# Kernel optimization log

Hardware: AMD Instinct MI355X
Metric: run time of the kernel (lower is better)

Reference implementation:

```python
import jax, jax.numpy as jnp
import numpy as np

N, E, R, D = 50000, 100000, 64, 50


def setup_inputs() -> dict:
    key = jax.random.key(0)
    k0, k1, k2, k3, k4 = jax.random.split(key, 5)
    h = jax.random.normal(k0, (N, D), dtype=jnp.float32)
    # xavier_uniform with gain=sqrt(2) (relu): bound = gain*sqrt(6/(fan_in+fan_out))
    bound = np.sqrt(2.0) * np.sqrt(6.0 / (D + D))
    weight = jax.random.uniform(k1, (R, D, D), dtype=jnp.float32, minval=-bound, maxval=bound)
    bias = jnp.ones((D,), dtype=jnp.float32)
    src_idx = jax.random.randint(k2, (E,), 0, N)
    dst_idx = jax.random.randint(k3, (E,), 0, N)
    rel_type = jax.random.randint(k4, (E,), 0, R)
    return {"h": h, "weight": weight, "bias": bias,
            "src_idx": src_idx, "dst_idx": dst_idx, "rel_type": rel_type}


def reference(h, weight, bias, src_idx, dst_idx, rel_type):
    # message_func: per-edge relation weight gather + bmm with source features
    # h[src_idx]: [E, D], weight[rel_type]: [E, D, D] -> msg: [E, D]
    msg = jnp.einsum('ed,edk->ek', h[src_idx], weight[rel_type])
    # sum-reduce messages onto destination nodes (DGL fn.sum semantics)
    agg = jax.ops.segment_sum(msg, dst_idx, num_segments=N)
    # apply_func: bias add + ReLU on node features
    return jax.nn.relu(agg + bias)
```

## Files before the change

kernel.cpp:

```cpp
#include <hip/hip_runtime.h>

#define NN 50000
#define DD 50
#define RR 64
#define BINS 2048
#define CAP 128
#define CAPN 24

#define BINCUR_OFF 0
#define DCUR_OFF   2048
#define PERM_OFF   52048
#define SD_OFF     1252048
#define META_INTS  1776336
#define WB_BYTE    ((size_t)META_INTS * 4)
#define MSG_BYTE   (WB_BYTE + (size_t)RR * 64 * 64 * 2)
#define WS_NEED    (MSG_BYTE + (size_t)BINS * CAP * 64 * 2)

typedef __attribute__((ext_vector_type(8))) short bf16x8;
typedef __attribute__((ext_vector_type(4))) float f32x4;

__device__ __forceinline__ unsigned short f2b(float f) {
    unsigned u = __float_as_uint(f);
    u = (u + 0x7fffu + ((u >> 16) & 1u)) >> 16;
    return (unsigned short)u;
}

__global__ __launch_bounds__(256) void k_zero(int* __restrict__ meta) {
    int i = blockIdx.x * 256 + threadIdx.x;
    if (i < BINS) meta[i] = 0;
}

__device__ __forceinline__ void load_a(const float* __restrict__ hrow, int ch,
                                       bf16x8& a0, bf16x8& a1) {
    const float2* hp0 = (const float2*)(hrow + ch * 8);
    float2 q0 = hp0[0], q1 = hp0[1], q2 = hp0[2], q3 = hp0[3];
    int kb = 32 + ch * 8;
    const float2 z2 = make_float2(0.f, 0.f);
    float2 q4 = (kb + 1 < DD) ? *(const float2*)(hrow + kb)     : z2;
    float2 q5 = (kb + 3 < DD) ? *(const float2*)(hrow + kb + 2) : z2;
    float2 q6 = (kb + 5 < DD) ? *(const float2*)(hrow + kb + 4) : z2;
    float2 q7 = (kb + 7 < DD) ? *(const float2*)(hrow + kb + 6) : z2;
    a0[0] = f2b(q0.x); a0[1] = f2b(q0.y); a0[2] = f2b(q1.x); a0[3] = f2b(q1.y);
    a0[4] = f2b(q2.x); a0[5] = f2b(q2.y); a0[6] = f2b(q3.x); a0[7] = f2b(q3.y);
    a1[0] = f2b(q4.x); a1[1] = f2b(q4.y); a1[2] = f2b(q5.x); a1[3] = f2b(q5.y);
    a1[4] = f2b(q6.x); a1[5] = f2b(q6.y); a1[6] = f2b(q7.x); a1[7] = f2b(q7.y);
}

__global__ __launch_bounds__(256) void k_prep(int* __restrict__ meta,
        unsigned short* __restrict__ wb, const float* __restrict__ w,
        const int* __restrict__ src, const int* __restrict__ dst,
        const int* __restrict__ rel, int E) {
    int tid = blockIdx.x * 256 + threadIdx.x;
    int nth = gridDim.x * 256;
    for (int j = tid; j < NN; j += nth) meta[DCUR_OFF + j] = 0;
    for (int j = tid; j < RR * 64 * 64; j += nth) {
        int r = j >> 12, d = (j >> 6) & 63, n = j & 63;
        float v = (n < DD && d < DD) ? w[r * (DD * DD) + d * DD + n] : 0.f;
        wb[(r << 12) + (n << 6) + d] = f2b(v);
    }
    for (int e = tid; e < E; e += nth) {
        int sb = (rel[e] << 5) | (e & 31);
        int p = atomicAdd(&meta[BINCUR_OFF + sb], 1);
        if (p < CAP)
            ((int2*)(meta + SD_OFF))[sb * CAP + p] = make_int2(src[e], dst[e]);
    }
}

__global__ __launch_bounds__(256) void k_edge(const float* __restrict__ h,
        const unsigned short* __restrict__ wb, int* __restrict__ meta,
        unsigned short* __restrict__ msg) {
    int lane = threadIdx.x & 63;
    int wv = (blockIdx.x << 2) + (threadIdx.x >> 6);
    int b = wv >> 2, qt = wv & 3;
    int r = b >> 5;
    int ch = lane >> 4, col0 = lane & 15;
    int slotbase = (b << 7) + (qt << 5);

    const unsigned short* wr = wb + ((size_t)r << 12) + (col0 << 6) + (ch << 3);
    bf16x8 bb0[4], bb1[4];
    #pragma unroll
    for (int t = 0; t < 4; ++t) {
        bb0[t] = *(const bf16x8*)(wr + t * 1024);
        bb1[t] = *(const bf16x8*)(wr + t * 1024 + 32);
    }

    int cnt = __builtin_amdgcn_readfirstlane(meta[BINCUR_OFF + b]);
    int2 sd = ((const int2*)(meta + SD_OFF))[slotbase + lane];
    if (cnt > CAP) cnt = CAP;
    int avail = cnt - (qt << 5);
    if (avail <= 0) return;
    if (avail > 32) avail = 32;

    int svx = (lane < avail) ? sd.x : 0;
    int sv0 = __shfl(svx, col0);
    int sv1 = __shfl(svx, 16 + col0);
    bf16x8 a00, a01, a10, a11;
    load_a(h + (size_t)sv0 * DD, ch, a00, a01);
    load_a(h + (size_t)sv1 * DD, ch, a10, a11);

    if (lane < avail) {
        int pos = atomicAdd(&meta[DCUR_OFF + sd.y], 1);
        if (pos < CAPN)
            meta[PERM_OFF + sd.y * CAPN + pos] = slotbase + lane;
    }

    {
        f32x4 c[4];
        #pragma unroll
        for (int t = 0; t < 4; ++t) {
            c[t] = (f32x4){0.f, 0.f, 0.f, 0.f};
            c[t] = __builtin_amdgcn_mfma_f32_16x16x32_bf16(a00, bb0[t], c[t], 0, 0, 0);
            c[t] = __builtin_amdgcn_mfma_f32_16x16x32_bf16(a01, bb1[t], c[t], 0, 0, 0);
        }
        unsigned short* mb = msg + (size_t)(slotbase + (ch << 2)) * 64;
        #pragma unroll
        for (int q = 0; q < 4; ++q)
            #pragma unroll
            for (int t = 0; t < 4; ++t)
                mb[q * 64 + t * 16 + col0] = f2b(c[t][q]);
    }
    if (avail > 16) {
        f32x4 c[4];
        #pragma unroll
        for (int t = 0; t < 4; ++t) {
            c[t] = (f32x4){0.f, 0.f, 0.f, 0.f};
            c[t] = __builtin_amdgcn_mfma_f32_16x16x32_bf16(a10, bb0[t], c[t], 0, 0, 0);
            c[t] = __builtin_amdgcn_mfma_f32_16x16x32_bf16(a11, bb1[t], c[t], 0, 0, 0);
        }
        unsigned short* mb = msg + (size_t)(slotbase + 16 + (ch << 2)) * 64;
        #pragma unroll
        for (int q = 0; q < 4; ++q)
            #pragma unroll
            for (int t = 0; t < 4; ++t)
                mb[q * 64 + t * 16 + col0] = f2b(c[t][q]);
    }
}

__global__ __launch_bounds__(256) void k_agg(const unsigned short* __restrict__ msg,
        const int* __restrict__ meta, const float* __restrict__ bias,
        float* __restrict__ out) {
    int lane = threadIdx.x & 63;
    int n0 = ((blockIdx.x << 2) + (threadIdx.x >> 6)) << 1;
    if (n0 >= NN) return;
    float bl = (lane < DD) ? bias[lane] : 0.f;
    #pragma unroll
    for (int ni = 0; ni < 2; ++ni) {
        int n = n0 + ni;
        if (n >= NN) break;
        int cnt = __builtin_amdgcn_readfirstlane(meta[DCUR_OFF + n]);
        if (cnt > CAPN) cnt = CAPN;
        float v = 0.f;
        const int4* pp = (const int4*)(meta + PERM_OFF + n * CAPN);
        int4 P0 = pp[0], P1 = pp[1];
        int pj[8] = {P0.x, P0.y, P0.z, P0.w, P1.x, P1.y, P1.z, P1.w};
        #pragma unroll
        for (int j = 0; j < 8; ++j) {
            if (j < cnt) {
                unsigned short u = msg[(size_t)pj[j] * 64 + lane];
                v += __uint_as_float((unsigned)u << 16);
            }
        }
        #pragma unroll 1
        for (int j = 8; j < cnt; ++j) {
            int p = meta[PERM_OFF + n * CAPN + j];
            unsigned short u = msg[(size_t)p * 64 + lane];
            v += __uint_as_float((unsigned)u << 16);
        }
        if (lane < DD) {
            float o = v + bl;
            out[(size_t)n * DD + lane] = o > 0.f ? o : 0.f;
        }
    }
}

__global__ void fb_edge_kernel(const float* __restrict__ h, const float* __restrict__ weight,
                               const int* __restrict__ src_idx, const int* __restrict__ dst_idx,
                               const int* __restrict__ rel_type, float* __restrict__ acc, int E) {
    int wave = (int)((blockIdx.x * blockDim.x + threadIdx.x) >> 6);
    int lane = threadIdx.x & 63;
    if (wave >= E) return;
    int s = src_idx[wave], r = rel_type[wave], dn = dst_idx[wave];
    const float* hs = h + (size_t)s * DD;
    const float* W  = weight + (size_t)r * DD * DD;
    if (lane < DD) {
        float m = 0.f;
        for (int d = 0; d < DD; ++d) m = fmaf(hs[d], W[d * DD + lane], m);
        atomicAdd(&acc[(size_t)dn * DD + lane], m);
    }
}
__global__ void fb_zero_kernel(float* __restrict__ out, int total) {
    int i = blockIdx.x * blockDim.x + threadIdx.x;
    if (i < total) out[i] = 0.f;
}
__global__ void fb_finalize_kernel(float* __restrict__ out, const float* __restrict__ bias, int total) {
    int i = blockIdx.x * blockDim.x + threadIdx.x;
    if (i < total) {
        float v = out[i] + bias[i % DD];
        out[i] = v > 0.f ? v : 0.f;
    }
}

extern "C" void kernel_launch(void* const* d_in, const int* in_sizes, int n_in,
                              void* d_out, int out_size, void* d_ws, size_t ws_size,
                              hipStream_t stream) {
    const float* h      = (const float*)d_in[0];
    const float* weight = (const float*)d_in[1];
    const float* bias   = (const float*)d_in[2];
    const int*   src    = (const int*)d_in[3];
    const int*   dst    = (const int*)d_in[4];
    const int*   rel    = (const int*)d_in[5];
    float* out = (float*)d_out;
    int E = in_sizes[3];

    if (ws_size >= WS_NEED) {
        int* meta = (int*)d_ws;
        unsigned short* wb  = (unsigned short*)((char*)d_ws + WB_BYTE);
        unsigned short* msg = (unsigned short*)((char*)d_ws + MSG_BYTE);

        k_zero<<<(BINS + 255) / 256, 256, 0, stream>>>(meta);
        k_prep<<<1024, 256, 0, stream>>>(meta, wb, weight, src, dst, rel, E);
        k_edge<<<2048, 256, 0, stream>>>(h, wb, meta, msg);
        k_agg<<<(NN + 7) / 8, 256, 0, stream>>>(msg, meta, bias, out);
    } else {
        fb_zero_kernel<<<(out_size + 255) / 256, 256, 0, stream>>>(out, out_size);
        fb_edge_kernel<<<(E + 3) / 4, 256, 0, stream>>>(h, weight, src, dst, rel, out, E);
        fb_finalize_kernel<<<(out_size + 255) / 256, 256, 0, stream>>>(out, bias, out_size);
    }
}
```

Before: 58.89 us.

## Scatter edge messages directly into per-destination slots, removing permutation indirection

The edge kernel now writes each message row straight into a destination-major buffer (dst*CAPN+pos) instead of writing to a bin-slot buffer and recording a permutation. The aggregation kernel then reads contiguous per-node message rows with no index lookup. The wave-to-bin mapping is also changed so that consecutive waves cover different bins, and the source-row gathers are issued before the count check to hide their latency. The cost is scattered 128-byte stores in the edge kernel and a much larger message buffer (NN*CAPN rows), which raises the workspace requirement.

```diff
diff --git a/kernel.cpp b/kernel.cpp
--- a/kernel.cpp
+++ b/kernel.cpp
@@ -9,12 +9,11 @@
 
 #define BINCUR_OFF 0
 #define DCUR_OFF   2048
-#define PERM_OFF   52048
-#define SD_OFF     1252048
-#define META_INTS  1776336
+#define SD_OFF     52048
+#define META_INTS  576336
 #define WB_BYTE    ((size_t)META_INTS * 4)
 #define MSG_BYTE   (WB_BYTE + (size_t)RR * 64 * 64 * 2)
-#define WS_NEED    (MSG_BYTE + (size_t)BINS * CAP * 64 * 2)
+#define WS_NEED    (MSG_BYTE + (size_t)NN * CAPN * 64 * 2)
 
 typedef __attribute__((ext_vector_type(8))) short bf16x8;
 typedef __attribute__((ext_vector_type(4))) float f32x4;
@@ -68,10 +67,10 @@
 
 __global__ __launch_bounds__(256) void k_edge(const float* __restrict__ h,
         const unsigned short* __restrict__ wb, int* __restrict__ meta,
-        unsigned short* __restrict__ msg) {
+        unsigned short* __restrict__ msgD) {
     int lane = threadIdx.x & 63;
     int wv = (blockIdx.x << 2) + (threadIdx.x >> 6);
-    int b = wv >> 2, qt = wv & 3;
+    int b = wv & (BINS - 1), qt = wv >> 11;
     int r = b >> 5;
     int ch = lane >> 4, col0 = lane & 15;
     int slotbase = (b << 7) + (qt << 5);
@@ -84,24 +83,23 @@
         bb1[t] = *(const bf16x8*)(wr + t * 1024 + 32);
     }
 
+    int2 sd = ((const int2*)(meta + SD_OFF))[slotbase + lane];
+    int svc = sd.x; svc = (svc < 0 || svc >= NN) ? 0 : svc;
+    int sv0 = __shfl(svc, col0);
+    int sv1 = __shfl(svc, 16 + col0);
+    bf16x8 a00, a01, a10, a11;
+    load_a(h + (size_t)sv0 * DD, ch, a00, a01);
+    load_a(h + (size_t)sv1 * DD, ch, a10, a11);
+
     int cnt = __builtin_amdgcn_readfirstlane(meta[BINCUR_OFF + b]);
-    int2 sd = ((const int2*)(meta + SD_OFF))[slotbase + lane];
     if (cnt > CAP) cnt = CAP;
     int avail = cnt - (qt << 5);
     if (avail <= 0) return;
     if (avail > 32) avail = 32;
 
-    int svx = (lane < avail) ? sd.x : 0;
-    int sv0 = __shfl(svx, col0);
-    int sv1 = __shfl(svx, 16 + col0);
-    bf16x8 a00, a01, a10, a11;
-    load_a(h + (size_t)sv0 * DD, ch, a00, a01);
-    load_a(h + (size_t)sv1 * DD, ch, a10, a11);
-
+    int pos = -1;
     if (lane < avail) {
-        int pos = atomicAdd(&meta[DCUR_OFF + sd.y], 1);
-        if (pos < CAPN)
-            meta[PERM_OFF + sd.y * CAPN + pos] = slotbase + lane;
+        pos = atomicAdd(&meta[DCUR_OFF + sd.y], 1);
     }
 
     {
@@ -112,12 +110,18 @@
             c[t] = __builtin_amdgcn_mfma_f32_16x16x32_bf16(a00, bb0[t], c[t], 0, 0, 0);
             c[t] = __builtin_amdgcn_mfma_f32_16x16x32_bf16(a01, bb1[t], c[t], 0, 0, 0);
         }
-        unsigned short* mb = msg + (size_t)(slotbase + (ch << 2)) * 64;
-        #pragma unroll
-        for (int q = 0; q < 4; ++q)
-            #pragma unroll
-            for (int t = 0; t < 4; ++t)
-                mb[q * 64 + t * 16 + col0] = f2b(c[t][q]);
+        #pragma unroll
+        for (int q = 0; q < 4; ++q) {
+            int rw = (ch << 2) + q;
+            int dvq  = __shfl(sd.y, rw);
+            int posq = __shfl(pos, rw);
+            if (rw < avail && posq >= 0 && posq < CAPN) {
+                unsigned short* mb = msgD + (size_t)(dvq * CAPN + posq) * 64;
+                #pragma unroll
+                for (int t = 0; t < 4; ++t)
+                    mb[t * 16 + col0] = f2b(c[t][q]);
+            }
+        }
     }
     if (avail > 16) {
         f32x4 c[4];
@@ -127,16 +131,22 @@
             c[t] = __builtin_amdgcn_mfma_f32_16x16x32_bf16(a10, bb0[t], c[t], 0, 0, 0);
             c[t] = __builtin_amdgcn_mfma_f32_16x16x32_bf16(a11, bb1[t], c[t], 0, 0, 0);
         }
-        unsigned short* mb = msg + (size_t)(slotbase + 16 + (ch << 2)) * 64;
-        #pragma unroll
-        for (int q = 0; q < 4; ++q)
-            #pragma unroll
-            for (int t = 0; t < 4; ++t)
-                mb[q * 64 + t * 16 + col0] = f2b(c[t][q]);
-    }
-}
-
-__global__ __launch_bounds__(256) void k_agg(const unsigned short* __restrict__ msg,
+        #pragma unroll
+        for (int q = 0; q < 4; ++q) {
+            int rw = 16 + (ch << 2) + q;
+            int dvq  = __shfl(sd.y, rw);
+            int posq = __shfl(pos, rw);
+            if (rw < avail && posq >= 0 && posq < CAPN) {
+                unsigned short* mb = msgD + (size_t)(dvq * CAPN + posq) * 64;
+                #pragma unroll
+                for (int t = 0; t < 4; ++t)
+                    mb[t * 16 + col0] = f2b(c[t][q]);
+            }
+        }
+    }
+}
+
+__global__ __launch_bounds__(256) void k_agg(const unsigned short* __restrict__ msgD,
         const int* __restrict__ meta, const float* __restrict__ bias,
         float* __restrict__ out) {
     int lane = threadIdx.x & 63;
@@ -149,21 +159,18 @@
         if (n >= NN) break;
         int cnt = __builtin_amdgcn_readfirstlane(meta[DCUR_OFF + n]);
         if (cnt > CAPN) cnt = CAPN;
+        const unsigned short* mb = msgD + (size_t)n * CAPN * 64 + lane;
         float v = 0.f;
-        const int4* pp = (const int4*)(meta + PERM_OFF + n * CAPN);
-        int4 P0 = pp[0], P1 = pp[1];
-        int pj[8] = {P0.x, P0.y, P0.z, P0.w, P1.x, P1.y, P1.z, P1.w};
         #pragma unroll
         for (int j = 0; j < 8; ++j) {
             if (j < cnt) {
-                unsigned short u = msg[(size_t)pj[j] * 64 + lane];
+                unsigned short u = mb[j * 64];
                 v += __uint_as_float((unsigned)u << 16);
             }
         }
         #pragma unroll 1
         for (int j = 8; j < cnt; ++j) {
-            int p = meta[PERM_OFF + n * CAPN + j];
-            unsigned short u = msg[(size_t)p * 64 + lane];
+            unsigned short u = mb[j * 64];
             v += __uint_as_float((unsigned)u << 16);
         }
         if (lane < DD) {
@@ -214,13 +221,13 @@
 
     if (ws_size >= WS_NEED) {
         int* meta = (int*)d_ws;
-        unsigned short* wb  = (unsigned short*)((char*)d_ws + WB_BYTE);
-        unsigned short* msg = (unsigned short*)((char*)d_ws + MSG_BYTE);
+        unsigned short* wb   = (unsigned short*)((char*)d_ws + WB_BYTE);
+        unsigned short* msgD = (unsigned short*)((char*)d_ws + MSG_BYTE);
 
         k_zero<<<(BINS + 255) / 256, 256, 0, stream>>>(meta);
         k_prep<<<1024, 256, 0, stream>>>(meta, wb, weight, src, dst, rel, E);
-        k_edge<<<2048, 256, 0, stream>>>(h, wb, meta, msg);
-        k_agg<<<(NN + 7) / 8, 256, 0, stream>>>(msg, meta, bias, out);
+        k_edge<<<2048, 256, 0, stream>>>(h, wb, meta, msgD);
+        k_agg<<<(NN + 7) / 8, 256, 0, stream>>>(msgD, meta, bias, out);
     } else {
         fb_zero_kernel<<<(out_size + 255) / 256, 256, 0, stream>>>(out, out_size);
         fb_edge_kernel<<<(E + 3) / 4, 256, 0, stream>>>(h, weight, src, dst, rel, out, E);
```

Measured after the change: 56.94 us. 3.3% less time.
